# Kernel optimization log

Hardware: AMD Instinct MI355X
Metric: run time of the kernel (lower is better)

The kernel has to match this reference:

```python
import jax, jax.numpy as jnp
import numpy as np

N_VER = 163842
IN_FEATS = 64
OUT_FEATS = 64


def setup_inputs() -> dict:
    key = jax.random.key(0)
    k1, k2, k3, k4 = jax.random.split(key, 4)
    x = jax.random.normal(k1, (N_VER, IN_FEATS), dtype=jnp.float32)
    hex_in = jax.random.randint(k2, (N_VER * 7,), 0, N_VER, dtype=jnp.int64)
    # Linear(7*in_feats, out_feats): weight stored as [7*in_feats, out_feats]
    W = jax.random.normal(k3, (7 * IN_FEATS, OUT_FEATS), dtype=jnp.float32) * (1.0 / np.sqrt(7 * IN_FEATS))
    b = jax.random.normal(k4, (OUT_FEATS,), dtype=jnp.float32) * 0.01
    return {"x": x, "hex_in": hex_in, "W": W, "b": b}


def reference(x, hex_in, W, b):
    n_ver = x.shape[0]
    # Gather 7-ring neighbor features: [7*n_ver, in_feats] -> [n_ver, 7*in_feats]
    x_new = x[hex_in].reshape(n_ver, 7 * x.shape[1])
    # Dense linear layer
    return x_new @ W + b
```

## Files before the change

### kernel.cpp

```cpp
#include <hip/hip_runtime.h>
#include <hip/hip_bf16.h>

#define N_VERT 163842
#define N8_X   1310736

typedef float  f32x4  __attribute__((ext_vector_type(4)));
typedef short  s16x8  __attribute__((ext_vector_type(8)));

__device__ __forceinline__ unsigned short f2bf(float f) {
  union { float f; unsigned int u; } c; c.f = f;
  unsigned int u = c.u;
  u += 0x7FFFu + ((u >> 16) & 1u);
  return (unsigned short)(u >> 16);
}

__device__ __forceinline__ s16x8 cvt8(const f32x4 a, const f32x4 b) {
  s16x8 h;
  h[0] = (short)f2bf(a[0]); h[1] = (short)f2bf(a[1]);
  h[2] = (short)f2bf(a[2]); h[3] = (short)f2bf(a[3]);
  h[4] = (short)f2bf(b[0]); h[5] = (short)f2bf(b[1]);
  h[6] = (short)f2bf(b[2]); h[7] = (short)f2bf(b[3]);
  return h;
}

__global__ void detect64(const unsigned int* __restrict__ hexw, int* __restrict__ flag) {
  __shared__ int any;
  if (threadIdx.x == 0) any = 0;
  __syncthreads();
  if (hexw[2 * threadIdx.x + 1] != 0u) any = 1;
  __syncthreads();
  if (threadIdx.x == 0) *flag = (any == 0) ? 1 : 0;
}

__global__ __launch_bounds__(256) void cvt_x_kernel(const float* __restrict__ x,
                                                    unsigned short* __restrict__ xbf) {
  int i = blockIdx.x * 256 + threadIdx.x;
  const int stride = gridDim.x * 256;
  for (; i < N8_X; i += stride) {
    const f32x4* s = (const f32x4*)(x + (size_t)i * 8);
    *(s16x8*)(xbf + (size_t)i * 8) = cvt8(s[0], s[1]);
  }
}

__global__ __launch_bounds__(256) void cvt_w_kernel(const float* __restrict__ W,
                                                    unsigned short* __restrict__ Wf) {
  const int t = blockIdx.x * 256 + threadIdx.x;
  if (t >= 448 * 64) return;
  const int e  = t & 7;
  const int ks = (t >> 3) % 14;
  const int c  = t / (14 * 8);
  const int hi = c >> 6, colc = c & 63;
  const int k  = ks * 32 + hi * 8 + e;
  Wf[t] = f2bf(W[k * 64 + colc]);
}

template <int BF>
__global__ __launch_bounds__(256, 4) void hexconv2(
    const void* __restrict__ xsrc,
    const unsigned int* __restrict__ hexw,
    const void* __restrict__ wsrc,
    const float* __restrict__ bias,
    float* __restrict__ out,
    const int* __restrict__ flag)
{
  __shared__ unsigned short Abuf[2][64 * 64];
  __shared__ unsigned int idxb[448];

  const int tid = threadIdx.x;
  const int wv  = tid >> 6;
  const int ln  = tid & 63;
  const int lo  = ln & 15;
  const int hi  = ln >> 4;
  const int vbase = blockIdx.x * 64;
  const int is64  = flag ? *flag : 1;

  const int col = (wv << 4) + lo;
  s16x8 bfrag[14];
  if (BF) {
    const s16x8* wf = (const s16x8*)wsrc + ((hi << 6) + col) * 14;
#pragma unroll
    for (int ks = 0; ks < 14; ++ks) bfrag[ks] = wf[ks];
  } else {
    const float* W = (const float*)wsrc;
#pragma unroll
    for (int ks = 0; ks < 14; ++ks) {
      const float* wp = W + (ks * 32 + hi * 8) * 64 + col;
      s16x8 bv;
#pragma unroll
      for (int e = 0; e < 8; ++e) bv[e] = (short)f2bf(wp[e * 64]);
      bfrag[ks] = bv;
    }
  }

  for (int g = tid; g < 448; g += 256) {
    unsigned int ib = 0;
    const int v = g / 7;
    if (vbase + v < N_VERT) {
      const long long r = (long long)vbase * 7 + g;
      const unsigned int idx = hexw[r << is64];
      ib = idx << (BF ? 7 : 8);
    }
    idxb[g] = ib;
  }
  __syncthreads();

  const int srow = tid >> 2, q = tid & 3;
  const unsigned int swz = (unsigned int)((srow & 7) << 4);
  char* myrow[2] = { (char*)&Abuf[0][0] + srow * 128,
                     (char*)&Abuf[1][0] + srow * 128 };
  const unsigned int wb0 = ((unsigned int)(q * 32))      ^ swz;
  const unsigned int wb1 = ((unsigned int)(q * 32 + 16)) ^ swz;
  const char* xbase = (const char*)xsrc;

  {
    const char* p = xbase + idxb[srow * 7] + (BF ? q * 32 : q * 64);
    s16x8 g0, g1;
    if (BF) {
      g0 = *(const s16x8*)p;
      g1 = *(const s16x8*)(p + 16);
    } else {
      const f32x4 r0 = *(const f32x4*)p,        r1 = *(const f32x4*)(p + 16);
      const f32x4 r2 = *(const f32x4*)(p + 32), r3 = *(const f32x4*)(p + 48);
      g0 = cvt8(r0, r1); g1 = cvt8(r2, r3);
    }
    *(s16x8*)(myrow[0] + wb0) = g0;
    *(s16x8*)(myrow[0] + wb1) = g1;
  }
  __syncthreads();

  f32x4 acc[4];
#pragma unroll
  for (int mt = 0; mt < 4; ++mt) acc[mt] = (f32x4){0.f, 0.f, 0.f, 0.f};

  const unsigned int rswz = (unsigned int)((lo & 7) << 4);

#pragma unroll
  for (int j = 0; j < 7; ++j) {
    const char* curbuf = (j & 1) ? (const char*)&Abuf[1][0] : (const char*)&Abuf[0][0];
    char* nxtrow = myrow[(j & 1) ^ 1];

    s16x8 g0, g1;
    f32x4 r0, r1, r2, r3;
    if (j < 6) {
      const char* p = xbase + idxb[srow * 7 + j + 1] + (BF ? q * 32 : q * 64);
      if (BF) {
        g0 = *(const s16x8*)p;
        g1 = *(const s16x8*)(p + 16);
      } else {
        r0 = *(const f32x4*)p;        r1 = *(const f32x4*)(p + 16);
        r2 = *(const f32x4*)(p + 32); r3 = *(const f32x4*)(p + 48);
      }
    }

#pragma unroll
    for (int kss = 0; kss < 2; ++kss) {
#pragma unroll
      for (int mt = 0; mt < 4; ++mt) {
        const int r = mt * 16 + lo;
        const s16x8 af = *(const s16x8*)(curbuf + r * 128 +
                           (((unsigned int)(kss * 64 + hi * 16)) ^ rswz));
        acc[mt] = __builtin_amdgcn_mfma_f32_16x16x32_bf16(af, bfrag[2 * j + kss], acc[mt], 0, 0, 0);
      }
    }

    if (j < 6) {
      if (!BF) { g0 = cvt8(r0, r1); g1 = cvt8(r2, r3); }
      *(s16x8*)(nxtrow + wb0) = g0;
      *(s16x8*)(nxtrow + wb1) = g1;
    }
    __syncthreads();
  }

  const float bval = bias[col];
#pragma unroll
  for (int mt = 0; mt < 4; ++mt) {
#pragma unroll
    for (int i = 0; i < 4; ++i) {
      const int row = vbase + mt * 16 + hi * 4 + i;
      if (row < N_VERT) out[(size_t)row * 64 + col] = acc[mt][i] + bval;
    }
  }
}

extern "C" void kernel_launch(void* const* d_in, const int* in_sizes, int n_in,
                              void* d_out, int out_size, void* d_ws, size_t ws_size,
                              hipStream_t stream) {
  const float*        x    = (const float*)d_in[0];
  const unsigned int* hexw = (const unsigned int*)d_in[1];
  const float*        W    = (const float*)d_in[2];
  const float*        b    = (const float*)d_in[3];
  float*              out  = (float*)d_out;

  const size_t WS_NEED = 65536 + (size_t)N_VERT * 64 * 2;
  int* flag = (ws_size >= 4) ? (int*)d_ws : nullptr;
  if (flag) detect64<<<1, 256, 0, stream>>>(hexw, flag);

  const int grid = (N_VERT + 63) / 64;

  if (flag && ws_size >= WS_NEED) {
    unsigned short* Wf  = (unsigned short*)((char*)d_ws + 4096);
    unsigned short* xbf = (unsigned short*)((char*)d_ws + 65536);
    cvt_w_kernel<<<(448 * 64 + 255) / 256, 256, 0, stream>>>(W, Wf);
    cvt_x_kernel<<<2048, 256, 0, stream>>>(x, xbf);
    hexconv2<1><<<grid, 256, 0, stream>>>(xbf, hexw, Wf, b, out, flag);
  } else {
    hexconv2<0><<<grid, 256, 0, stream>>>(x, hexw, W, b, out, flag);
  }
}
```

Measured before the change: 55.91 us.

## Fuse prep kernels and restructure hexconv to direct-register A gathers with LDS weights

Merges the index-width detection, weight conversion and x-to-bf16 conversion into a single prep kernel, which cuts the launch count. The main kernel now processes 256 rows per 512-thread block. Each wave gathers its A fragments for 32 rows straight from global memory into registers, double-buffered across the 7 neighbor slots, so the LDS staging buffer and the per-step barriers are gone. The bf16 weights are staged once per block in LDS and read from there for the B operand. This trades more LDS and fewer blocks for fewer barriers and a larger tile per wave, and it relies on the uncoalesced direct gathers being tolerable.

```diff
diff --git a/kernel.cpp b/kernel.cpp
--- a/kernel.cpp
+++ b/kernel.cpp
@@ -1,8 +1,9 @@
 #include <hip/hip_runtime.h>
-#include <hip/hip_bf16.h>
 
 #define N_VERT 163842
 #define N8_X   1310736
+#define RPB    256
+#define GRID_MAIN ((N_VERT + RPB - 1) / RPB)
 
 typedef float  f32x4  __attribute__((ext_vector_type(4)));
 typedef short  s16x8  __attribute__((ext_vector_type(8)));
@@ -32,30 +33,39 @@
   if (threadIdx.x == 0) *flag = (any == 0) ? 1 : 0;
 }
 
-__global__ __launch_bounds__(256) void cvt_x_kernel(const float* __restrict__ x,
-                                                    unsigned short* __restrict__ xbf) {
-  int i = blockIdx.x * 256 + threadIdx.x;
+__global__ __launch_bounds__(256) void prep(
+    const float* __restrict__ x, const unsigned int* __restrict__ hexw,
+    const float* __restrict__ W,
+    unsigned short* __restrict__ Wf, unsigned short* __restrict__ xbf,
+    int* __restrict__ flag)
+{
+  const int b = blockIdx.x, tid = threadIdx.x;
+
+  if (b == 0) {
+    __shared__ int any;
+    if (tid == 0) any = 0;
+    __syncthreads();
+    if (hexw[2 * tid + 1] != 0u) any = 1;
+    __syncthreads();
+    if (tid == 0) *flag = (any == 0) ? 1 : 0;
+  }
+  if (b >= 1 && b <= 112) {
+    const int t   = (b - 1) * 256 + tid;
+    const int e   = t & 7;
+    const int col = (t >> 3) & 63;
+    const int hi  = (t >> 9) & 3;
+    const int ks  = t >> 11;
+    Wf[t] = f2bf(W[(ks * 32 + hi * 8 + e) * 64 + col]);
+  }
   const int stride = gridDim.x * 256;
-  for (; i < N8_X; i += stride) {
+  for (int i = b * 256 + tid; i < N8_X; i += stride) {
     const f32x4* s = (const f32x4*)(x + (size_t)i * 8);
     *(s16x8*)(xbf + (size_t)i * 8) = cvt8(s[0], s[1]);
   }
 }
 
-__global__ __launch_bounds__(256) void cvt_w_kernel(const float* __restrict__ W,
-                                                    unsigned short* __restrict__ Wf) {
-  const int t = blockIdx.x * 256 + threadIdx.x;
-  if (t >= 448 * 64) return;
-  const int e  = t & 7;
-  const int ks = (t >> 3) % 14;
-  const int c  = t / (14 * 8);
-  const int hi = c >> 6, colc = c & 63;
-  const int k  = ks * 32 + hi * 8 + e;
-  Wf[t] = f2bf(W[k * 64 + colc]);
-}
-
 template <int BF>
-__global__ __launch_bounds__(256, 4) void hexconv2(
+__global__ __launch_bounds__(512, 4) void hexconv3(
     const void* __restrict__ xsrc,
     const unsigned int* __restrict__ hexw,
     const void* __restrict__ wsrc,
@@ -63,121 +73,119 @@
     float* __restrict__ out,
     const int* __restrict__ flag)
 {
-  __shared__ unsigned short Abuf[2][64 * 64];
-  __shared__ unsigned int idxb[448];
+  __shared__ unsigned short Wl[28672];
+  __shared__ unsigned int   offb[RPB * 7];
 
   const int tid = threadIdx.x;
   const int wv  = tid >> 6;
   const int ln  = tid & 63;
   const int lo  = ln & 15;
   const int hi  = ln >> 4;
-  const int vbase = blockIdx.x * 64;
+  const int vbase = blockIdx.x * RPB;
   const int is64  = flag ? *flag : 1;
 
-  const int col = (wv << 4) + lo;
-  s16x8 bfrag[14];
   if (BF) {
-    const s16x8* wf = (const s16x8*)wsrc + ((hi << 6) + col) * 14;
-#pragma unroll
-    for (int ks = 0; ks < 14; ++ks) bfrag[ks] = wf[ks];
+    const s16x8* wsv = (const s16x8*)wsrc;
+#pragma unroll
+    for (int it = 0; it < 7; ++it)
+      ((s16x8*)Wl)[it * 512 + tid] = wsv[it * 512 + tid];
   } else {
     const float* W = (const float*)wsrc;
-#pragma unroll
-    for (int ks = 0; ks < 14; ++ks) {
-      const float* wp = W + (ks * 32 + hi * 8) * 64 + col;
-      s16x8 bv;
-#pragma unroll
-      for (int e = 0; e < 8; ++e) bv[e] = (short)f2bf(wp[e * 64]);
-      bfrag[ks] = bv;
-    }
-  }
-
-  for (int g = tid; g < 448; g += 256) {
-    unsigned int ib = 0;
-    const int v = g / 7;
-    if (vbase + v < N_VERT) {
-      const long long r = (long long)vbase * 7 + g;
-      const unsigned int idx = hexw[r << is64];
-      ib = idx << (BF ? 7 : 8);
-    }
-    idxb[g] = ib;
+    for (int it = 0; it < 56; ++it) {
+      const int t   = it * 512 + tid;
+      const int e   = t & 7;
+      const int col = (t >> 3) & 63;
+      const int hif = (t >> 9) & 3;
+      const int ks  = t >> 11;
+      Wl[t] = f2bf(W[(ks * 32 + hif * 8 + e) * 64 + col]);
+    }
+  }
+
+#pragma unroll
+  for (int it = 0; it < 4; ++it) {
+    const int g = it * 512 + tid;
+    if (g < RPB * 7) {
+      unsigned int ib = 0;
+      const int v = g / 7;
+      if (vbase + v < N_VERT) {
+        const unsigned int r = (unsigned int)vbase * 7 + g;
+        ib = hexw[r << is64] << (BF ? 7 : 8);
+      }
+      offb[g] = ib;
+    }
   }
   __syncthreads();
 
-  const int srow = tid >> 2, q = tid & 3;
-  const unsigned int swz = (unsigned int)((srow & 7) << 4);
-  char* myrow[2] = { (char*)&Abuf[0][0] + srow * 128,
-                     (char*)&Abuf[1][0] + srow * 128 };
-  const unsigned int wb0 = ((unsigned int)(q * 32))      ^ swz;
-  const unsigned int wb1 = ((unsigned int)(q * 32 + 16)) ^ swz;
+  const int r0 = wv * 32 + lo, r1 = r0 + 16;
+  unsigned int off0[7], off1[7];
+#pragma unroll
+  for (int j = 0; j < 7; ++j) { off0[j] = offb[r0 * 7 + j]; off1[j] = offb[r1 * 7 + j]; }
+
   const char* xbase = (const char*)xsrc;
-
-  {
-    const char* p = xbase + idxb[srow * 7] + (BF ? q * 32 : q * 64);
-    s16x8 g0, g1;
-    if (BF) {
-      g0 = *(const s16x8*)p;
-      g1 = *(const s16x8*)(p + 16);
-    } else {
-      const f32x4 r0 = *(const f32x4*)p,        r1 = *(const f32x4*)(p + 16);
-      const f32x4 r2 = *(const f32x4*)(p + 32), r3 = *(const f32x4*)(p + 48);
-      g0 = cvt8(r0, r1); g1 = cvt8(r2, r3);
-    }
-    *(s16x8*)(myrow[0] + wb0) = g0;
-    *(s16x8*)(myrow[0] + wb1) = g1;
-  }
-  __syncthreads();
-
-  f32x4 acc[4];
-#pragma unroll
-  for (int mt = 0; mt < 4; ++mt) acc[mt] = (f32x4){0.f, 0.f, 0.f, 0.f};
-
-  const unsigned int rswz = (unsigned int)((lo & 7) << 4);
+  const char* Wb    = (const char*)Wl + (hi * 64 + lo) * 16;
+
+  f32x4 acc0[4], acc1[4];
+#pragma unroll
+  for (int nt = 0; nt < 4; ++nt) { acc0[nt] = (f32x4){0,0,0,0}; acc1[nt] = (f32x4){0,0,0,0}; }
+
+  s16x8 a[2][2][2];
+#define LOAD_A(par, jj)                                                        \
+  do {                                                                         \
+    const char* p0 = xbase + off0[jj];                                         \
+    const char* p1 = xbase + off1[jj];                                         \
+    if (BF) {                                                                  \
+      a[par][0][0] = *(const s16x8*)(p0 + hi * 16);                            \
+      a[par][1][0] = *(const s16x8*)(p0 + 64 + hi * 16);                       \
+      a[par][0][1] = *(const s16x8*)(p1 + hi * 16);                            \
+      a[par][1][1] = *(const s16x8*)(p1 + 64 + hi * 16);                       \
+    } else {                                                                   \
+      const f32x4* q0 = (const f32x4*)(p0 + hi * 32);                          \
+      const f32x4* q1 = (const f32x4*)(p1 + hi * 32);                          \
+      a[par][0][0] = cvt8(q0[0], q0[1]);                                       \
+      a[par][1][0] = cvt8(*(const f32x4*)(p0 + 128 + hi * 32),                 \
+                          *(const f32x4*)(p0 + 144 + hi * 32));                \
+      a[par][0][1] = cvt8(q1[0], q1[1]);                                       \
+      a[par][1][1] = cvt8(*(const f32x4*)(p1 + 128 + hi * 32),                 \
+                          *(const f32x4*)(p1 + 144 + hi * 32));                \
+    }                                                                          \
+  } while (0)
+
+  LOAD_A(0, 0);
 
 #pragma unroll
   for (int j = 0; j < 7; ++j) {
-    const char* curbuf = (j & 1) ? (const char*)&Abuf[1][0] : (const char*)&Abuf[0][0];
-    char* nxtrow = myrow[(j & 1) ^ 1];
-
-    s16x8 g0, g1;
-    f32x4 r0, r1, r2, r3;
-    if (j < 6) {
-      const char* p = xbase + idxb[srow * 7 + j + 1] + (BF ? q * 32 : q * 64);
-      if (BF) {
-        g0 = *(const s16x8*)p;
-        g1 = *(const s16x8*)(p + 16);
-      } else {
-        r0 = *(const f32x4*)p;        r1 = *(const f32x4*)(p + 16);
-        r2 = *(const f32x4*)(p + 32); r3 = *(const f32x4*)(p + 48);
+    const int cur = j & 1, nxt = cur ^ 1;
+    if (j < 6) LOAD_A(nxt, j + 1);
+#pragma unroll
+    for (int kss = 0; kss < 2; ++kss) {
+#pragma unroll
+      for (int nt = 0; nt < 4; ++nt) {
+        const s16x8 bf = *(const s16x8*)(Wb + (2 * j + kss) * 4096 + nt * 256);
+        acc0[nt] = __builtin_amdgcn_mfma_f32_16x16x32_bf16(a[cur][kss][0], bf, acc0[nt], 0, 0, 0);
+        acc1[nt] = __builtin_amdgcn_mfma_f32_16x16x32_bf16(a[cur][kss][1], bf, acc1[nt], 0, 0, 0);
       }
     }
-
-#pragma unroll
-    for (int kss = 0; kss < 2; ++kss) {
-#pragma unroll
-      for (int mt = 0; mt < 4; ++mt) {
-        const int r = mt * 16 + lo;
-        const s16x8 af = *(const s16x8*)(curbuf + r * 128 +
-                           (((unsigned int)(kss * 64 + hi * 16)) ^ rswz));
-        acc[mt] = __builtin_amdgcn_mfma_f32_16x16x32_bf16(af, bfrag[2 * j + kss], acc[mt], 0, 0, 0);
-      }
-    }
-
-    if (j < 6) {
-      if (!BF) { g0 = cvt8(r0, r1); g1 = cvt8(r2, r3); }
-      *(s16x8*)(nxtrow + wb0) = g0;
-      *(s16x8*)(nxtrow + wb1) = g1;
-    }
-    __syncthreads();
-  }
-
-  const float bval = bias[col];
-#pragma unroll
-  for (int mt = 0; mt < 4; ++mt) {
-#pragma unroll
-    for (int i = 0; i < 4; ++i) {
-      const int row = vbase + mt * 16 + hi * 4 + i;
-      if (row < N_VERT) out[(size_t)row * 64 + col] = acc[mt][i] + bval;
+  }
+#undef LOAD_A
+
+  float bval[4];
+#pragma unroll
+  for (int nt = 0; nt < 4; ++nt) bval[nt] = bias[nt * 16 + lo];
+
+  const int rbase = vbase + wv * 32;
+#pragma unroll
+  for (int i = 0; i < 4; ++i) {
+    const int row0 = rbase + hi * 4 + i;
+    if (row0 < N_VERT) {
+      float* orow = out + (size_t)row0 * 64;
+#pragma unroll
+      for (int nt = 0; nt < 4; ++nt) orow[nt * 16 + lo] = acc0[nt][i] + bval[nt];
+    }
+    const int row1 = rbase + 16 + hi * 4 + i;
+    if (row1 < N_VERT) {
+      float* orow = out + (size_t)row1 * 64;
+#pragma unroll
+      for (int nt = 0; nt < 4; ++nt) orow[nt * 16 + lo] = acc1[nt][i] + bval[nt];
     }
   }
 }
@@ -192,18 +200,16 @@
   float*              out  = (float*)d_out;
 
   const size_t WS_NEED = 65536 + (size_t)N_VERT * 64 * 2;
-  int* flag = (ws_size >= 4) ? (int*)d_ws : nullptr;
-  if (flag) detect64<<<1, 256, 0, stream>>>(hexw, flag);
-
-  const int grid = (N_VERT + 63) / 64;
-
-  if (flag && ws_size >= WS_NEED) {
-    unsigned short* Wf  = (unsigned short*)((char*)d_ws + 4096);
-    unsigned short* xbf = (unsigned short*)((char*)d_ws + 65536);
-    cvt_w_kernel<<<(448 * 64 + 255) / 256, 256, 0, stream>>>(W, Wf);
-    cvt_x_kernel<<<2048, 256, 0, stream>>>(x, xbf);
-    hexconv2<1><<<grid, 256, 0, stream>>>(xbf, hexw, Wf, b, out, flag);
+
+  if (ws_size >= WS_NEED) {
+    int*            flag = (int*)d_ws;
+    unsigned short* Wf   = (unsigned short*)((char*)d_ws + 4096);
+    unsigned short* xbf  = (unsigned short*)((char*)d_ws + 65536);
+    prep<<<2048, 256, 0, stream>>>(x, hexw, W, Wf, xbf, flag);
+    hexconv3<1><<<GRID_MAIN, 512, 0, stream>>>(xbf, hexw, Wf, b, out, flag);
   } else {
-    hexconv2<0><<<grid, 256, 0, stream>>>(x, hexw, W, b, out, flag);
-  }
-}
+    int* flag = (ws_size >= 4) ? (int*)d_ws : nullptr;
+    if (flag) detect64<<<1, 256, 0, stream>>>(hexw, flag);
+    hexconv3<0><<<GRID_MAIN, 512, 0, stream>>>(x, hexw, W, b, out, flag);
+  }
+}
```

After: 45.58 us. -18.5%, faster.
